# Kernel optimization log

Hardware: AMD Instinct MI355X
Metric: run time of the kernel (lower is better)

Reference implementation:

```python
import jax, jax.numpy as jnp
import numpy as np

COMMITMENT_COST = 0.25
NUM_EMBEDDINGS = 1024
EMBEDDING_DIM = 256


def setup_inputs() -> dict:
    key = jax.random.key(0)
    k1, k2 = jax.random.split(key)
    inputs = jax.random.normal(k1, (32, 32, 32, EMBEDDING_DIM), dtype=jnp.float32)
    # GlorotUniform-ish init for the [D, K] codebook
    limit = float(np.sqrt(6.0 / (EMBEDDING_DIM + NUM_EMBEDDINGS)))
    w = jax.random.uniform(k2, (EMBEDDING_DIM, NUM_EMBEDDINGS), dtype=jnp.float32,
                           minval=-limit, maxval=limit)
    return {"inputs": inputs, "w": w}


def reference(inputs, w):
    D, K = w.shape
    flat = inputs.reshape(-1, D)                                   # [N, D]
    distances = (jnp.sum(flat * flat, axis=1, keepdims=True)
                 - 2.0 * (flat @ w)
                 + jnp.sum(w * w, axis=0, keepdims=True))          # [N, K]
    enc_idx_flat = jnp.argmin(distances, axis=1)                   # [N]
    encodings = jax.nn.one_hot(enc_idx_flat, K, dtype=inputs.dtype)  # [N, K]
    encoding_indices = enc_idx_flat.reshape(inputs.shape[:-1])     # [B, H, W]
    quantized = jnp.take(w.T, encoding_indices, axis=0)            # [B, H, W, D]

    e_latent_loss = jnp.mean((jax.lax.stop_gradient(quantized) - inputs) ** 2)
    q_latent_loss = jnp.mean((quantized - jax.lax.stop_gradient(inputs)) ** 2)
    loss = q_latent_loss + COMMITMENT_COST * e_latent_loss

    quantized_skip = inputs + jax.lax.stop_gradient(quantized - inputs)

    avg_probs = jnp.mean(encodings, axis=0)                        # [K]
    perplexity = jnp.exp(-jnp.sum(avg_probs * jnp.log(avg_probs + 1e-10)))
    return (quantized_skip, loss, perplexity, encodings, encoding_indices)
```

## Files before the change

### kernel.cpp

```cpp
#include <hip/hip_runtime.h>
#include <cfloat>
#include <cmath>
#include <stdint.h>

#define NROWS 32768
#define DIM   256
#define KC    1024

typedef short bf16x8 __attribute__((ext_vector_type(8)));
typedef float f32x4  __attribute__((ext_vector_type(4)));
typedef float f32x2  __attribute__((ext_vector_type(2)));

__device__ inline unsigned short f2bf(float f) {
    unsigned u = __float_as_uint(f);
    u = (u + 0x7fffu + ((u >> 16) & 1u)) >> 16;
    return (unsigned short)u;
}

__global__ __launch_bounds__(256) void prep_w(const float* __restrict__ w,
                                              uint4* __restrict__ wph,
                                              float* __restrict__ wT) {
    const int t = blockIdx.x * 256 + threadIdx.x;
    const int l = t & 63;
    const int ks = (t >> 6) & 7;
    const int ctg = t >> 9;
    const int c = ctg * 16 + (l & 15);
    const int kbase = ks * 32 + ((l >> 4) << 3);
    union { unsigned short u[8]; uint4 v; } H;
#pragma unroll
    for (int j = 0; j < 8; ++j) {
        float v = w[(size_t)(kbase + j) * KC + c];
        H.u[j] = f2bf(v);
        wT[(size_t)c * DIM + kbase + j] = v;
    }
    wph[t] = H.v;
}

__global__ __launch_bounds__(256) void wnorm_kernel(const float* __restrict__ wT,
                                                    double* __restrict__ wnorm64,
                                                    float* __restrict__ wnormf) {
    const int k = blockIdx.x * 256 + threadIdx.x;
    const float* p = wT + (size_t)k * DIM;
    double acc = 0.0;
#pragma unroll 8
    for (int d = 0; d < DIM; ++d) acc += (double)p[d] * (double)p[d];
    wnorm64[k] = acc;
    wnormf[k] = (float)acc;
}

__global__ __launch_bounds__(256, 4) void vq_screen(
    const float* __restrict__ x,
    const char* __restrict__ wph,
    const float* __restrict__ wnormf,
    int* __restrict__ cand,
    float* __restrict__ out_enc)
{
    __shared__ char ldsbuf[32768];

    const int t = threadIdx.x;
    const int l = t & 63;
    const int wv = t >> 6;
    const int p = blockIdx.x & 1;
    const int rt = blockIdx.x >> 1;
    const int r0 = rt * 64 + wv * 16;
    const size_t pbase = (size_t)p * 262144;

    bf16x8 ah[8];
    {
        const float* xb = x + (size_t)(r0 + (l & 15)) * DIM + ((l >> 4) << 3);
#pragma unroll
        for (int ks = 0; ks < 8; ++ks) {
            float4 p0 = *(const float4*)(xb + ks * 32);
            float4 p1 = *(const float4*)(xb + ks * 32 + 4);
            float f[8] = {p0.x, p0.y, p0.z, p0.w, p1.x, p1.y, p1.z, p1.w};
            union { unsigned short u[8]; bf16x8 v; } H;
#pragma unroll
            for (int j = 0; j < 8; ++j) H.u[j] = f2bf(f[j]);
            ah[ks] = H.v;
        }
    }

    float tv0[4], tv1[4], tv2[4];
    int   tk0[4], tk1[4], tk2[4];
#pragma unroll
    for (int r = 0; r < 4; ++r) { tv0[r] = tv1[r] = tv2[r] = FLT_MAX; tk0[r] = tk1[r] = tk2[r] = 0; }

    {
        const char* g0 = wph + pbase + wv * 4096 + l * 16;
        char* lp0 = ldsbuf + wv * 4096 + l * 16;
#pragma unroll
        for (int i = 0; i < 4; ++i)
            __builtin_amdgcn_global_load_lds(
                (const __attribute__((address_space(1))) void*)(g0 + i * 1024),
                (__attribute__((address_space(3))) void*)(lp0 + i * 1024), 16, 0, 0);
    }
    __syncthreads();

    int cur = 0;
    for (int g = 0; g < 16; ++g) {
        if (g + 1 < 16) {
            const char* gp = wph + pbase + (size_t)(g + 1) * 16384 + wv * 4096 + l * 16;
            char* lp = ldsbuf + (cur ^ 1) * 16384 + wv * 4096 + l * 16;
#pragma unroll
            for (int i = 0; i < 4; ++i)
                __builtin_amdgcn_global_load_lds(
                    (const __attribute__((address_space(1))) void*)(gp + i * 1024),
                    (__attribute__((address_space(3))) void*)(lp + i * 1024), 16, 0, 0);
        }

        {
            const int zrow = r0 + g;
            f32x2* er2 = (f32x2*)(out_enc + (size_t)zrow * KC + p * 512);
            f32x2 z = {0.f, 0.f};
#pragma unroll
            for (int i = 0; i < 4; ++i)
                __builtin_nontemporal_store(z, er2 + i * 64 + l);
        }

        f32x4 acc[2];
#pragma unroll
        for (int ct = 0; ct < 2; ++ct) acc[ct] = (f32x4){0.f, 0.f, 0.f, 0.f};

#pragma unroll
        for (int ks = 0; ks < 8; ++ks) {
#pragma unroll
            for (int ct = 0; ct < 2; ++ct) {
                bf16x8 bh = *(const bf16x8*)(ldsbuf + cur * 16384 + ((ct * 8 + ks) * 64 + l) * 16);
                acc[ct] = __builtin_amdgcn_mfma_f32_16x16x32_bf16(ah[ks], bh, acc[ct], 0, 0, 0);
            }
        }

#pragma unroll
        for (int ct = 0; ct < 2; ++ct) {
            const int k = (p * 32 + g * 2 + ct) * 16 + (l & 15);
            const float wn = wnormf[k];
#pragma unroll
            for (int r = 0; r < 4; ++r) {
                float s = wn - 2.0f * acc[ct][r];
                if (s < tv2[r]) {
                    if (s < tv1[r]) {
                        tv2[r] = tv1[r]; tk2[r] = tk1[r];
                        if (s < tv0[r]) { tv1[r] = tv0[r]; tk1[r] = tk0[r]; tv0[r] = s; tk0[r] = k; }
                        else            { tv1[r] = s;      tk1[r] = k; }
                    } else { tv2[r] = s; tk2[r] = k; }
                }
            }
        }

        if (g + 1 < 16) __syncthreads();
        cur ^= 1;
    }

    const float margin = 0.125f;
    const int grpShift = (l >> 4) * 16;
    const unsigned laneMask = (1u << (l & 15)) - 1u;
#pragma unroll
    for (int r = 0; r < 4; ++r) {
        float v = tv0[r];
#pragma unroll
        for (int m = 1; m <= 8; m <<= 1) v = fminf(v, __shfl_xor(v, m));
        const float thr = v + margin;
        const int row = r0 + ((l >> 4) << 2) + r;
        int* creg = cand + ((size_t)row * 2 + p) * 16;
        int base = 0;
        {
            bool c = tv0[r] <= thr;
            unsigned long long bal = __ballot(c);
            unsigned grp = (unsigned)(bal >> grpShift) & 0xFFFFu;
            int pos = base + __popc(grp & laneMask);
            if (c && pos < 7) { creg[1 + pos] = tk0[r]; creg[8 + pos] = __float_as_int(tv0[r]); }
            base += __popc(grp);
        }
        {
            bool c = tv1[r] <= thr;
            unsigned long long bal = __ballot(c);
            unsigned grp = (unsigned)(bal >> grpShift) & 0xFFFFu;
            int pos = base + __popc(grp & laneMask);
            if (c && pos < 7) { creg[1 + pos] = tk1[r]; creg[8 + pos] = __float_as_int(tv1[r]); }
            base += __popc(grp);
        }
        {
            bool c = tv2[r] <= thr;
            unsigned long long bal = __ballot(c);
            unsigned grp = (unsigned)(bal >> grpShift) & 0xFFFFu;
            int pos = base + __popc(grp & laneMask);
            if (c && pos < 7) { creg[1 + pos] = tk2[r]; creg[8 + pos] = __float_as_int(tv2[r]); }
            base += __popc(grp);
        }
        if ((l & 15) == 0) creg[0] = base < 7 ? base : 7;
    }
}

__global__ __launch_bounds__(256) void vq_final(
    const float* __restrict__ x, const float* __restrict__ wT,
    const double* __restrict__ wnorm64,
    const int* __restrict__ cand,
    float* __restrict__ out_q, float* __restrict__ out_idx, float* __restrict__ out_enc,
    int* __restrict__ counts, double* __restrict__ loss_sum)
{
    const int t = threadIdx.x;
    const int l = t & 63;
    const int wv = t >> 6;
    __shared__ double wsum[4];
    const float margin = 0.125f;

    double ls0 = 0.0, ls1 = 0.0, ls2 = 0.0, ls3 = 0.0;
    const int stride = gridDim.x * 4;
    for (int row = blockIdx.x * 4 + wv; row < NROWS; row += stride) {
        const float4 xv = ((const float4*)(x + (size_t)row * DIM))[l];
        const int* c0 = cand + (size_t)row * 32;

        float m = FLT_MAX;
#pragma unroll
        for (int p2 = 0; p2 < 2; ++p2) {
            const int* cp = c0 + p2 * 16;
            const int n = cp[0];
            for (int c = 0; c < n; ++c) m = fminf(m, __int_as_float(cp[8 + c]));
        }
        const float thr = m + margin;

        int bk = 0x7FFFFFFF, cnt = 0;
#pragma unroll
        for (int p2 = 0; p2 < 2; ++p2) {
            const int* cp = c0 + p2 * 16;
            const int n = cp[0];
            for (int c = 0; c < n; ++c)
                if (__int_as_float(cp[8 + c]) <= thr) { ++cnt; bk = cp[1 + c]; }
        }
        if (cnt > 1) {
            double best = 1e300; bk = 0x7FFFFFFF;
#pragma unroll
            for (int p2 = 0; p2 < 2; ++p2) {
                const int* cp = c0 + p2 * 16;
                const int n = cp[0];
                for (int c = 0; c < n; ++c) {
                    if (__int_as_float(cp[8 + c]) > thr) continue;
                    const int k2 = cp[1 + c];
                    const float4 w4 = ((const float4*)(wT + (size_t)k2 * DIM))[l];
                    double d = (double)xv.x * (double)w4.x;
                    d = fma((double)xv.y, (double)w4.y, d);
                    d = fma((double)xv.z, (double)w4.z, d);
                    d = fma((double)xv.w, (double)w4.w, d);
#pragma unroll
                    for (int mm = 32; mm > 0; mm >>= 1) d += __shfl_xor(d, mm);
                    const double s64 = wnorm64[k2] - 2.0 * d;
                    if (s64 < best || (s64 == best && k2 < bk)) { best = s64; bk = k2; }
                }
            }
        }
        const int k = __builtin_amdgcn_readfirstlane(bk);

        const float4 qv = ((const float4*)(wT + (size_t)k * DIM))[l];
        f32x4 o = {xv.x + (qv.x - xv.x), xv.y + (qv.y - xv.y),
                   xv.z + (qv.z - xv.z), xv.w + (qv.w - xv.w)};
        __builtin_nontemporal_store(o, (f32x4*)(out_q + (size_t)row * DIM) + l);
        double dx = (double)qv.x - (double)xv.x; ls0 = fma(dx, dx, ls0);
        dx = (double)qv.y - (double)xv.y; ls1 = fma(dx, dx, ls1);
        dx = (double)qv.z - (double)xv.z; ls2 = fma(dx, dx, ls2);
        dx = (double)qv.w - (double)xv.w; ls3 = fma(dx, dx, ls3);
        if (l == 0) {
            out_enc[(size_t)row * KC + k] = 1.0f;
            out_idx[row] = (float)k;
            atomicAdd(&counts[k], 1);
        }
    }
    double lsum = (ls0 + ls1) + (ls2 + ls3);
#pragma unroll
    for (int off = 32; off > 0; off >>= 1) lsum += __shfl_down(lsum, off);
    if (l == 0) wsum[wv] = lsum;
    __syncthreads();
    if (t == 0) atomicAdd(loss_sum, wsum[0] + wsum[1] + wsum[2] + wsum[3]);
}

__global__ __launch_bounds__(1024) void final_kernel(const int* __restrict__ counts,
                                                     const double* __restrict__ loss_sum,
                                                     float* __restrict__ out_loss,
                                                     float* __restrict__ out_ppl) {
    const int t = threadIdx.x;
    double p = (double)counts[t] * (1.0 / 32768.0);
    double term = -p * log(p + 1e-10);
#pragma unroll
    for (int off = 32; off > 0; off >>= 1) term += __shfl_down(term, off);
    __shared__ double ws[16];
    if ((t & 63) == 0) ws[t >> 6] = term;
    __syncthreads();
    if (t == 0) {
        double s = 0.0;
        for (int i = 0; i < 16; ++i) s += ws[i];
        *out_ppl = (float)exp(s);
        *out_loss = (float)(1.25 * loss_sum[0] * (1.0 / 8388608.0));
    }
}

extern "C" void kernel_launch(void* const* d_in, const int* in_sizes, int n_in,
                              void* d_out, int out_size, void* d_ws, size_t ws_size,
                              hipStream_t stream) {
    const float* x = (const float*)d_in[0];
    const float* w = (const float*)d_in[1];

    float* out = (float*)d_out;
    float* out_q    = out;
    float* out_loss = out + 8388608;
    float* out_ppl  = out + 8388609;
    float* out_enc  = out + 8388610;
    float* out_idx  = out + 8388610 + 33554432;

    char* wsb = (char*)d_ws;
    double* loss_sum = (double*)(wsb + 0);
    int*    counts   = (int*)(wsb + 64);
    double* wnorm64  = (double*)(wsb + 4160);
    float*  wnormf   = (float*)(wsb + 12352);
    float*  wT       = (float*)(wsb + 16448);
    uint4*  wph      = (uint4*)(wsb + 1065024);
    int*    cand     = (int*)(wsb + 1589312);

    (void)hipMemsetAsync(d_ws, 0, 4160, stream);

    prep_w<<<128, 256, 0, stream>>>(w, wph, wT);
    wnorm_kernel<<<4, 256, 0, stream>>>(wT, wnorm64, wnormf);
    vq_screen<<<1024, 256, 0, stream>>>(x, (const char*)wph, wnormf, cand, out_enc);
    vq_final<<<2048, 256, 0, stream>>>(x, wT, wnorm64, cand,
                                       out_q, out_idx, out_enc, counts, loss_sum);
    final_kernel<<<1, 1024, 0, stream>>>(counts, loss_sum, out_loss, out_ppl);
}
```

Baseline: 132.6 us.

## Fuse weight prep with norms and screen with final via ticket handoff

Merges the codebook norm computation into the bf16 packing kernel, using a shuffle and LDS reduction in place of a separate per-row double loop. It also merges the screening and final refinement kernels: each pair of blocks covering the same 64-row tile increments a ticket, and the second block to finish does the candidate resolution and output writes for those rows. This removes two kernel launches and the global round trip between stages. In exchange, the final pass now runs on only half the blocks at the tail of each tile, which can lower parallelism in that phase and add atomics and fences.

```diff
diff --git a/kernel.cpp b/kernel.cpp
--- a/kernel.cpp
+++ b/kernel.cpp
@@ -6,6 +6,7 @@
 #define NROWS 32768
 #define DIM   256
 #define KC    1024
+#define MARGIN 0.125f
 
 typedef short bf16x8 __attribute__((ext_vector_type(8)));
 typedef float f32x4  __attribute__((ext_vector_type(4)));
@@ -17,45 +18,54 @@
     return (unsigned short)u;
 }
 
-__global__ __launch_bounds__(256) void prep_w(const float* __restrict__ w,
-                                              uint4* __restrict__ wph,
-                                              float* __restrict__ wT) {
-    const int t = blockIdx.x * 256 + threadIdx.x;
-    const int l = t & 63;
-    const int ks = (t >> 6) & 7;
-    const int ctg = t >> 9;
+__global__ __launch_bounds__(512) void prep_wnorm(const float* __restrict__ w,
+                                                  uint4* __restrict__ wph,
+                                                  float* __restrict__ wT,
+                                                  double* __restrict__ wnorm64,
+                                                  float* __restrict__ wnormf) {
+    const int tl = threadIdx.x;
+    const int ctg = blockIdx.x;
+    const int t = ctg * 512 + tl;
+    const int l = tl & 63;
+    const int ks = (tl >> 6) & 7;
     const int c = ctg * 16 + (l & 15);
     const int kbase = ks * 32 + ((l >> 4) << 3);
     union { unsigned short u[8]; uint4 v; } H;
+    double s = 0.0;
 #pragma unroll
     for (int j = 0; j < 8; ++j) {
         float v = w[(size_t)(kbase + j) * KC + c];
         H.u[j] = f2bf(v);
         wT[(size_t)c * DIM + kbase + j] = v;
+        s = fma((double)v, (double)v, s);
     }
     wph[t] = H.v;
-}
-
-__global__ __launch_bounds__(256) void wnorm_kernel(const float* __restrict__ wT,
-                                                    double* __restrict__ wnorm64,
-                                                    float* __restrict__ wnormf) {
-    const int k = blockIdx.x * 256 + threadIdx.x;
-    const float* p = wT + (size_t)k * DIM;
-    double acc = 0.0;
-#pragma unroll 8
-    for (int d = 0; d < DIM; ++d) acc += (double)p[d] * (double)p[d];
-    wnorm64[k] = acc;
-    wnormf[k] = (float)acc;
-}
-
-__global__ __launch_bounds__(256, 4) void vq_screen(
+    s += __shfl_xor(s, 16);
+    s += __shfl_xor(s, 32);
+    __shared__ double part[8][16];
+    if (l < 16) part[ks][l] = s;
+    __syncthreads();
+    if (tl < 16) {
+        double tot = 0.0;
+#pragma unroll
+        for (int i = 0; i < 8; ++i) tot += part[i][tl];
+        wnorm64[ctg * 16 + tl] = tot;
+        wnormf[ctg * 16 + tl] = (float)tot;
+    }
+}
+
+__global__ __launch_bounds__(256, 4) void vq_fused(
     const float* __restrict__ x,
     const char* __restrict__ wph,
-    const float* __restrict__ wnormf,
-    int* __restrict__ cand,
-    float* __restrict__ out_enc)
+    const float* __restrict__ wT,
+    const double* __restrict__ wnorm64, const float* __restrict__ wnormf,
+    int* __restrict__ cand, int* __restrict__ ticket,
+    float* __restrict__ out_q, float* __restrict__ out_idx, float* __restrict__ out_enc,
+    int* __restrict__ counts, double* __restrict__ loss_sum)
 {
     __shared__ char ldsbuf[32768];
+    __shared__ int sh_tick;
+    __shared__ double wsum[4];
 
     const int t = threadIdx.x;
     const int l = t & 63;
@@ -151,7 +161,6 @@
         cur ^= 1;
     }
 
-    const float margin = 0.125f;
     const int grpShift = (l >> 4) * 16;
     const unsigned laneMask = (1u << (l & 15)) - 1u;
 #pragma unroll
@@ -159,7 +168,7 @@
         float v = tv0[r];
 #pragma unroll
         for (int m = 1; m <= 8; m <<= 1) v = fminf(v, __shfl_xor(v, m));
-        const float thr = v + margin;
+        const float thr = v + MARGIN;
         const int row = r0 + ((l >> 4) << 2) + r;
         int* creg = cand + ((size_t)row * 2 + p) * 16;
         int base = 0;
@@ -189,24 +198,17 @@
         }
         if ((l & 15) == 0) creg[0] = base < 7 ? base : 7;
     }
-}
-
-__global__ __launch_bounds__(256) void vq_final(
-    const float* __restrict__ x, const float* __restrict__ wT,
-    const double* __restrict__ wnorm64,
-    const int* __restrict__ cand,
-    float* __restrict__ out_q, float* __restrict__ out_idx, float* __restrict__ out_enc,
-    int* __restrict__ counts, double* __restrict__ loss_sum)
-{
-    const int t = threadIdx.x;
-    const int l = t & 63;
-    const int wv = t >> 6;
-    __shared__ double wsum[4];
-    const float margin = 0.125f;
+
+    __threadfence();
+    __syncthreads();
+    if (t == 0) sh_tick = atomicAdd(&ticket[rt], 1);
+    __syncthreads();
+    if (sh_tick != 1) return;
+    __threadfence();
 
     double ls0 = 0.0, ls1 = 0.0, ls2 = 0.0, ls3 = 0.0;
-    const int stride = gridDim.x * 4;
-    for (int row = blockIdx.x * 4 + wv; row < NROWS; row += stride) {
+    for (int rr = 0; rr < 16; ++rr) {
+        const int row = rt * 64 + wv * 16 + rr;
         const float4 xv = ((const float4*)(x + (size_t)row * DIM))[l];
         const int* c0 = cand + (size_t)row * 32;
 
@@ -217,7 +219,7 @@
             const int n = cp[0];
             for (int c = 0; c < n; ++c) m = fminf(m, __int_as_float(cp[8 + c]));
         }
-        const float thr = m + margin;
+        const float thr = m + MARGIN;
 
         int bk = 0x7FFFFFFF, cnt = 0;
 #pragma unroll
@@ -308,18 +310,18 @@
     char* wsb = (char*)d_ws;
     double* loss_sum = (double*)(wsb + 0);
     int*    counts   = (int*)(wsb + 64);
-    double* wnorm64  = (double*)(wsb + 4160);
-    float*  wnormf   = (float*)(wsb + 12352);
-    float*  wT       = (float*)(wsb + 16448);
-    uint4*  wph      = (uint4*)(wsb + 1065024);
-    int*    cand     = (int*)(wsb + 1589312);
-
-    (void)hipMemsetAsync(d_ws, 0, 4160, stream);
-
-    prep_w<<<128, 256, 0, stream>>>(w, wph, wT);
-    wnorm_kernel<<<4, 256, 0, stream>>>(wT, wnorm64, wnormf);
-    vq_screen<<<1024, 256, 0, stream>>>(x, (const char*)wph, wnormf, cand, out_enc);
-    vq_final<<<2048, 256, 0, stream>>>(x, wT, wnorm64, cand,
+    int*    ticket   = (int*)(wsb + 4160);
+    double* wnorm64  = (double*)(wsb + 6208);
+    float*  wnormf   = (float*)(wsb + 14400);
+    float*  wT       = (float*)(wsb + 18496);
+    uint4*  wph      = (uint4*)(wsb + 1067072);
+    int*    cand     = (int*)(wsb + 1591360);
+
+    (void)hipMemsetAsync(d_ws, 0, 6208, stream);
+
+    prep_wnorm<<<64, 512, 0, stream>>>(w, wph, wT, wnorm64, wnormf);
+    vq_fused<<<1024, 256, 0, stream>>>(x, (const char*)wph, wT, wnorm64, wnormf,
+                                       cand, ticket,
                                        out_q, out_idx, out_enc, counts, loss_sum);
     final_kernel<<<1, 1024, 0, stream>>>(counts, loss_sum, out_loss, out_ppl);
 }
```

Result: slower. 361.5 us (+172.7%).
